# Optimization experiments

Hardware: AMD Instinct MI355X
Metric: run time of the kernel (lower is better)

Reference implementation:

```python
import math
import jax, jax.numpy as jnp
from jax import lax
import numpy as np

L, B, S, H, N = 2, 1, 2048, 1024, 16
HN = H // N
EPS = 1e-5
SIGMA = 0.02
OUT_STD = SIGMA / math.sqrt(2.0 * L)


def gelu(x):
    # OpenAI tanh-approx gelu, matching gelu_impl
    return 0.5 * x * (1.0 + jnp.tanh(0.7978845608028654 * x * (1.0 + 0.044715 * x * x)))


def layer_norm(x, g, b):
    mu = jnp.mean(x, axis=-1, keepdims=True)
    var = jnp.mean(jnp.square(x - mu), axis=-1, keepdims=True)
    return (x - mu) / jnp.sqrt(var + EPS) * g + b


def setup_inputs() -> dict:
    key = jax.random.key(0)
    ks = jax.random.split(key, 8)
    x = jax.random.normal(ks[0], (B, S, H), dtype=jnp.float32)
    ltor_mask = jnp.tril(jnp.ones((S, S), dtype=jnp.float32))[None, None]  # [1,1,S,S]
    return {
        "hidden_states": x,
        "ltor_mask": ltor_mask,
        "ln1_g": jnp.ones((L, H), jnp.float32),
        "ln1_b": jnp.zeros((L, H), jnp.float32),
        "qkv_w": jax.random.normal(ks[1], (L, H, 3 * H), jnp.float32) * SIGMA,
        "qkv_b": jnp.zeros((L, 3 * H), jnp.float32),
        "dense_w": jax.random.normal(ks[2], (L, H, H), jnp.float32) * OUT_STD,
        "dense_b": jnp.zeros((L, H), jnp.float32),
        "ln2_g": jnp.ones((L, H), jnp.float32),
        "ln2_b": jnp.zeros((L, H), jnp.float32),
        "fc_w": jax.random.normal(ks[3], (L, H, 4 * H), jnp.float32) * SIGMA,
        "fc_b": jnp.zeros((L, 4 * H), jnp.float32),
        "proj_w": jax.random.normal(ks[4], (L, 4 * H, H), jnp.float32) * OUT_STD,
        "proj_b": jnp.zeros((L, H), jnp.float32),
        "lnf_g": jnp.ones((H,), jnp.float32),
        "lnf_b": jnp.zeros((H,), jnp.float32),
    }


def _transformer(hidden_states, ltor_mask, ln1_g, ln1_b, qkv_w, qkv_b, dense_w, dense_b,
                 ln2_g, ln2_b, fc_w, fc_b, proj_w, proj_b, lnf_g, lnf_b):
    scale = 1.0 / math.sqrt(HN)

    def step(h, p):
        g1, b1, qw, qb, dw, db, g2, b2, fw, fb, pw, pb = p
        y = layer_norm(h, g1, b1)
        qkv = y @ qw + qb                       # [B,S,3H]
        q, k, v = jnp.split(qkv, 3, axis=-1)
        # [B,S,H] -> [B,N,S,HN]
        q = q.reshape(B, S, N, HN).transpose(0, 2, 1, 3)
        k = k.reshape(B, S, N, HN).transpose(0, 2, 1, 3)
        v = v.reshape(B, S, N, HN).transpose(0, 2, 1, 3)
        scores = jnp.einsum('bnqd,bnkd->bnqk', q, k) * scale
        scores = scores * ltor_mask - 10000.0 * (1.0 - ltor_mask)
        probs = jax.nn.softmax(scores, axis=-1)
        ctx = jnp.einsum('bnqk,bnkd->bnqd', probs, v)
        ctx = ctx.transpose(0, 2, 1, 3).reshape(B, S, H)
        attn_out = ctx @ dw + db
        h2 = h + attn_out
        y2 = layer_norm(h2, g2, b2)
        mlp_out = gelu(y2 @ fw + fb) @ pw + pb
        return h2 + mlp_out, None

    params = (ln1_g, ln1_b, qkv_w, qkv_b, dense_w, dense_b,
              ln2_g, ln2_b, fc_w, fc_b, proj_w, proj_b)
    h, _ = lax.scan(step, hidden_states, params)
    return layer_norm(h, lnf_g, lnf_b)


def reference(hidden_states, ltor_mask, ln1_g, ln1_b, qkv_w, qkv_b, dense_w, dense_b,
              ln2_g, ln2_b, fc_w, fc_b, proj_w, proj_b, lnf_g, lnf_b):
    return _transformer(hidden_states, ltor_mask, ln1_g, ln1_b, qkv_w, qkv_b,
                        dense_w, dense_b, ln2_g, ln2_b, fc_w, fc_b,
                        proj_w, proj_b, lnf_g, lnf_b)
```

## Files before the change

kernel.cpp:

```cpp
#include <hip/hip_runtime.h>
#include <hip/hip_bf16.h>
#include <cstdint>
#include <cstddef>

typedef __bf16 bf16;
typedef __attribute__((ext_vector_type(4))) __bf16 bf16x4;
typedef __attribute__((ext_vector_type(8))) __bf16 bf16x8;
typedef __attribute__((ext_vector_type(4))) float floatx4;

__device__ __forceinline__ void gload16(const bf16* g, bf16* l) {
    __builtin_amdgcn_global_load_lds(
        (const __attribute__((address_space(1))) void*)g,
        (__attribute__((address_space(3))) void*)l, 16, 0, 0);
}

__global__ __launch_bounds__(256) void ln_first(const float* __restrict__ x,
                                                float* __restrict__ h,
                                                const float* __restrict__ g,
                                                const float* __restrict__ b,
                                                bf16* __restrict__ y) {
    __shared__ float red[8];
    const int row = blockIdx.x, tid = threadIdx.x;
    const size_t off = (size_t)row * 1024 + tid * 4;
    const float4 v = *(const float4*)(x + off);
    *(float4*)(h + off) = v;
    float s = v.x + v.y + v.z + v.w;
#pragma unroll
    for (int o = 32; o > 0; o >>= 1) s += __shfl_xor(s, o);
    if ((tid & 63) == 0) red[tid >> 6] = s;
    __syncthreads();
    const float mean = (red[0] + red[1] + red[2] + red[3]) * (1.f / 1024.f);
    const float d[4] = {v.x - mean, v.y - mean, v.z - mean, v.w - mean};
    float q = d[0] * d[0] + d[1] * d[1] + d[2] * d[2] + d[3] * d[3];
#pragma unroll
    for (int o = 32; o > 0; o >>= 1) q += __shfl_xor(q, o);
    if ((tid & 63) == 0) red[4 + (tid >> 6)] = q;
    __syncthreads();
    const float var = (red[4] + red[5] + red[6] + red[7]) * (1.f / 1024.f);
    const float rstd = rsqrtf(var + 1e-5f);
    const int base = tid * 4;
#pragma unroll
    for (int i = 0; i < 4; i++)
        y[off + i] = (bf16)(d[i] * rstd * g[base + i] + b[base + i]);
}

template <typename OutT, int KS>
__global__ __launch_bounds__(256) void reduce_ln(const bf16* __restrict__ part,
                                                 const float* __restrict__ bias,
                                                 float* __restrict__ h,
                                                 const float* __restrict__ g,
                                                 const float* __restrict__ b,
                                                 OutT* __restrict__ y) {
    __shared__ float red[8];
    const int row = blockIdx.x, tid = threadIdx.x;
    const int base = tid * 4;
    const size_t off = (size_t)row * 1024 + base;
    const float4 hv = *(const float4*)(h + off);
    const float4 bv = *(const float4*)(bias + base);
    float a[4] = {hv.x + bv.x, hv.y + bv.y, hv.z + bv.z, hv.w + bv.w};
#pragma unroll
    for (int z = 0; z < KS; z++) {
        bf16x4 pv = *(const bf16x4*)(part + (size_t)z * (2048 * 1024) + off);
#pragma unroll
        for (int i = 0; i < 4; i++) a[i] += (float)pv[i];
    }
    *(float4*)(h + off) = (float4){a[0], a[1], a[2], a[3]};
    float s = a[0] + a[1] + a[2] + a[3];
#pragma unroll
    for (int o = 32; o > 0; o >>= 1) s += __shfl_xor(s, o);
    if ((tid & 63) == 0) red[tid >> 6] = s;
    __syncthreads();
    const float mean = (red[0] + red[1] + red[2] + red[3]) * (1.f / 1024.f);
    const float d[4] = {a[0] - mean, a[1] - mean, a[2] - mean, a[3] - mean};
    float q = d[0] * d[0] + d[1] * d[1] + d[2] * d[2] + d[3] * d[3];
#pragma unroll
    for (int o = 32; o > 0; o >>= 1) q += __shfl_xor(q, o);
    if ((tid & 63) == 0) red[4 + (tid >> 6)] = q;
    __syncthreads();
    const float var = (red[4] + red[5] + red[6] + red[7]) * (1.f / 1024.f);
    const float rstd = rsqrtf(var + 1e-5f);
#pragma unroll
    for (int i = 0; i < 4; i++)
        y[off + i] = (OutT)(d[i] * rstd * g[base + i] + b[base + i]);
}

__global__ __launch_bounds__(256) void transpose_all(const float* __restrict__ qkv_w,
                                                     const float* __restrict__ dense_w,
                                                     const float* __restrict__ fc_w,
                                                     const float* __restrict__ proj_w,
                                                     bf16* __restrict__ wT) {
    __shared__ bf16 T[128][72];
    int b = blockIdx.x;
    const int layer = (b >= 1536) ? 1 : 0;
    b -= layer * 1536;
    const float* src; bf16* dst; int K, N, kx, ny;
    bf16* wl = wT + (size_t)layer * 12582912;
    if (b < 384)       { src = qkv_w  + (size_t)layer * 1024 * 3072; dst = wl;            K = 1024; N = 3072; kx = b & 7;  ny = b >> 3; }
    else if (b < 512)  { b -= 384;  src = dense_w + (size_t)layer * 1024 * 1024; dst = wl + 3145728; K = 1024; N = 1024; kx = b & 7;  ny = b >> 3; }
    else if (b < 1024) { b -= 512;  src = fc_w    + (size_t)layer * 1024 * 4096; dst = wl + 4194304; K = 1024; N = 4096; kx = b & 7;  ny = b >> 3; }
    else               { b -= 1024; src = proj_w  + (size_t)layer * 4096 * 1024; dst = wl + 8388608; K = 4096; N = 1024; kx = b & 31; ny = b >> 5; }
    const int k0 = kx * 128, n0 = ny * 64;
    {
        const int r = threadIdx.x >> 4;
        const int c4 = (threadIdx.x & 15) * 4;
#pragma unroll
        for (int j = 0; j < 8; j++) {
            const int kk = r + j * 16;
            float4 v = *(const float4*)&src[(size_t)(k0 + kk) * N + n0 + c4];
            bf16x4 bv; bv[0] = (bf16)v.x; bv[1] = (bf16)v.y; bv[2] = (bf16)v.z; bv[3] = (bf16)v.w;
            *(bf16x4*)&T[kk][c4 ^ (((kk >> 5) & 3) << 4)] = bv;
        }
    }
    __syncthreads();
    {
        const int n = threadIdx.x >> 2;
        const int kc = (threadIdx.x & 3) * 32;
#pragma unroll
        for (int j = 0; j < 4; j++) {
            bf16x8 v;
#pragma unroll
            for (int i = 0; i < 8; i++) {
                const int k = kc + j * 8 + i;
                v[i] = T[k][n ^ (((k >> 5) & 3) << 4)];
            }
            *(bf16x8*)&dst[(size_t)(n0 + n) * K + k0 + kc + j * 8] = v;
        }
    }
}

template <int MODE>
__global__ __launch_bounds__(256) void gemm_bt64(const bf16* __restrict__ A,
                                                 const bf16* __restrict__ BT,
                                                 const float* __restrict__ bias,
                                                 bf16* __restrict__ outb,
                                                 int M, int N, int K) {
    __shared__ bf16 As[64 * 64];
    __shared__ bf16 Bs[128 * 64];
    const int tid = threadIdx.x;
    const int w = tid >> 6, lane = tid & 63;
    const int quad = lane >> 4, l16 = lane & 15;
    const int wm = w >> 1, wn = w & 1;
    const int m0 = blockIdx.x * 64, n0 = blockIdx.y * 128;
    const int kchunk = K / gridDim.z;
    const int kbeg = blockIdx.z * kchunk;

    const int srow = lane >> 3;
    const int scol = ((lane & 7) ^ srow) * 8;
    const bf16* ga = A + (size_t)(m0 + w * 16 + srow) * K + kbeg + scol;
    const bf16* gb = BT + (size_t)(n0 + w * 32 + srow) * K + kbeg + scol;
    bf16* la = As + (w * 16) * 64;
    bf16* lb = Bs + (w * 32) * 64;

    floatx4 acc[2][4];
#pragma unroll
    for (int i = 0; i < 2; i++)
#pragma unroll
        for (int j = 0; j < 4; j++) acc[i][j] = (floatx4){0.f, 0.f, 0.f, 0.f};

#pragma unroll
    for (int s = 0; s < 2; s++) gload16(ga + (size_t)(s * 8) * K, la + s * 8 * 64);
#pragma unroll
    for (int s = 0; s < 4; s++) gload16(gb + (size_t)(s * 8) * K, lb + s * 8 * 64);

    const int xq = (l16 & 7) * 8;

    for (int kk = 0; kk < kchunk; kk += 64) {
        __syncthreads();
        bf16x8 af[2][2], bfr[2][4];
#pragma unroll
        for (int ks = 0; ks < 2; ks++) {
            const int colz = (ks * 32 + quad * 8) ^ xq;
#pragma unroll
            for (int i = 0; i < 2; i++)
                af[ks][i]  = *(const bf16x8*)&As[(wm * 32 + i * 16 + l16) * 64 + colz];
#pragma unroll
            for (int i = 0; i < 4; i++)
                bfr[ks][i] = *(const bf16x8*)&Bs[(wn * 64 + i * 16 + l16) * 64 + colz];
        }
        __syncthreads();
        if (kk + 64 < kchunk) {
#pragma unroll
            for (int s = 0; s < 2; s++) gload16(ga + (size_t)(s * 8) * K + kk + 64, la + s * 8 * 64);
#pragma unroll
            for (int s = 0; s < 4; s++) gload16(gb + (size_t)(s * 8) * K + kk + 64, lb + s * 8 * 64);
        }
#pragma unroll
        for (int ks = 0; ks < 2; ks++)
#pragma unroll
            for (int ms = 0; ms < 2; ms++)
#pragma unroll
                for (int ns = 0; ns < 4; ns++)
                    acc[ms][ns] = __builtin_amdgcn_mfma_f32_16x16x32_bf16(af[ks][ms], bfr[ks][ns],
                                                                          acc[ms][ns], 0, 0, 0);
    }

    bf16* pout = (MODE == 2) ? (outb + (size_t)blockIdx.z * M * N) : outb;
#pragma unroll
    for (int ms = 0; ms < 2; ms++) {
#pragma unroll
        for (int ns = 0; ns < 4; ns++) {
            const int row = m0 + wm * 32 + ms * 16 + quad * 4;
            const int col = n0 + wn * 64 + ns * 16 + l16;
            const float bv = (MODE == 2) ? 0.f : bias[col];
#pragma unroll
            for (int i = 0; i < 4; i++) {
                float v = acc[ms][ns][i] + bv;
                size_t idx = (size_t)(row + i) * N + col;
                if (MODE == 1) {
                    float t = 0.7978845608028654f * v * (1.f + 0.044715f * v * v);
                    pout[idx] = (bf16)(0.5f * v * (1.f + tanhf(t)));
                } else {
                    pout[idx] = (bf16)v;
                }
            }
        }
    }
}

__global__ __launch_bounds__(256) void attn_mfma(const bf16* __restrict__ qkv,
                                                 bf16* __restrict__ ctx) {
    __shared__ bf16 Ks[64][68];
    __shared__ bf16 Vt[64][72];
    __shared__ bf16 QPa[64][68];
    __shared__ bf16 QPb[64][68];
    const int tid = threadIdx.x;
    const int w = tid >> 6, lane = tid & 63;
    const int quad = lane >> 4, l16 = lane & 15;
    const int head = blockIdx.y;
    const int qta = blockIdx.x;
    const int qtb = 31 - qta;
    const int qa = qta * 64, qb = qtb * 64;
    const int rowg = w * 16 + quad * 4;
    const int r = tid >> 2;
    const int c = (tid & 3) * 16;
    const float SC = 0.18033688011111827f;

    {
        const bf16* pa = qkv + (size_t)(qa + r) * 3072 + head * 64 + c;
        const bf16* pb = qkv + (size_t)(qb + r) * 3072 + head * 64 + c;
        bf16x8 a0 = *(const bf16x8*)pa, a1 = *(const bf16x8*)(pa + 8);
        bf16x8 b0 = *(const bf16x8*)pb, b1 = *(const bf16x8*)(pb + 8);
        bf16x8 sa0, sa1, sb0, sb1;
#pragma unroll
        for (int i = 0; i < 8; i++) {
            sa0[i] = (bf16)((float)a0[i] * SC); sa1[i] = (bf16)((float)a1[i] * SC);
            sb0[i] = (bf16)((float)b0[i] * SC); sb1[i] = (bf16)((float)b1[i] * SC);
        }
        *(bf16x8*)&QPa[r][c] = sa0; *(bf16x8*)&QPa[r][c + 8] = sa1;
        *(bf16x8*)&QPb[r][c] = sb0; *(bf16x8*)&QPb[r][c + 8] = sb1;
    }
    const bf16x8 aqA0 = *(const bf16x8*)&QPa[w * 16 + l16][quad * 8];
    const bf16x8 aqA1 = *(const bf16x8*)&QPa[w * 16 + l16][32 + quad * 8];
    const bf16x8 aqB0 = *(const bf16x8*)&QPb[w * 16 + l16][quad * 8];
    const bf16x8 aqB1 = *(const bf16x8*)&QPb[w * 16 + l16][32 + quad * 8];

    float lsa[4] = {0.f, 0.f, 0.f, 0.f}, lsb[4] = {0.f, 0.f, 0.f, 0.f};
    floatx4 oa[4], ob[4];
#pragma unroll
    for (int d = 0; d < 4; d++) {
        oa[d] = (floatx4){0.f, 0.f, 0.f, 0.f};
        ob[d] = (floatx4){0.f, 0.f, 0.f, 0.f};
    }

    const int nt = qtb + 1;
    bf16x8 kr0, kr1, vr0, vr1;
    {
        const bf16* kp = qkv + (size_t)r * 3072 + 1024 + head * 64 + c;
        kr0 = *(const bf16x8*)kp; kr1 = *(const bf16x8*)(kp + 8);
        const bf16* vp = qkv + (size_t)lane * 3072 + 2048 + head * 64 + w * 16;
        vr0 = *(const bf16x8*)vp; vr1 = *(const bf16x8*)(vp + 8);
    }

    for (int t = 0; t < nt; t++) {
        __syncthreads();
        *(bf16x8*)&Ks[r][c] = kr0;
        *(bf16x8*)&Ks[r][c + 8] = kr1;
#pragma unroll
        for (int i = 0; i < 8; i++) {
            Vt[w * 16 + i][lane] = vr0[i];
            Vt[w * 16 + 8 + i][lane] = vr1[i];
        }
        __syncthreads();
        if (t + 1 < nt) {
            const size_t kb = (size_t)(t + 1) * 64;
            const bf16* kp = qkv + (kb + r) * 3072 + 1024 + head * 64 + c;
            kr0 = *(const bf16x8*)kp; kr1 = *(const bf16x8*)(kp + 8);
            const bf16* vp = qkv + (kb + lane) * 3072 + 2048 + head * 64 + w * 16;
            vr0 = *(const bf16x8*)vp; vr1 = *(const bf16x8*)(vp + 8);
        }
        const bool doA = (t <= qta);

        floatx4 s4b[4], s4a[4];
#pragma unroll
        for (int n = 0; n < 4; n++) s4b[n] = (floatx4){0.f, 0.f, 0.f, 0.f};
#pragma unroll
        for (int n = 0; n < 4; n++) {
            bf16x8 bk0 = *(const bf16x8*)&Ks[n * 16 + l16][quad * 8];
            bf16x8 bk1 = *(const bf16x8*)&Ks[n * 16 + l16][32 + quad * 8];
            s4b[n] = __builtin_amdgcn_mfma_f32_16x16x32_bf16(aqB0, bk0, s4b[n], 0, 0, 0);
            s4b[n] = __builtin_amdgcn_mfma_f32_16x16x32_bf16(aqB1, bk1, s4b[n], 0, 0, 0);
        }
        if (doA) {
#pragma unroll
            for (int n = 0; n < 4; n++) s4a[n] = (floatx4){0.f, 0.f, 0.f, 0.f};
#pragma unroll
            for (int n = 0; n < 4; n++) {
                bf16x8 bk0 = *(const bf16x8*)&Ks[n * 16 + l16][quad * 8];
                bf16x8 bk1 = *(const bf16x8*)&Ks[n * 16 + l16][32 + quad * 8];
                s4a[n] = __builtin_amdgcn_mfma_f32_16x16x32_bf16(aqA0, bk0, s4a[n], 0, 0, 0);
                s4a[n] = __builtin_amdgcn_mfma_f32_16x16x32_bf16(aqA1, bk1, s4a[n], 0, 0, 0);
            }
        }

        {
            float p[4][4];
            if (t == nt - 1) {
#pragma unroll
                for (int i = 0; i < 4; i++)
#pragma unroll
                    for (int n = 0; n < 4; n++)
                        p[n][i] = (n * 16 + l16 > rowg + i) ? 0.f
                                  : __builtin_amdgcn_exp2f(s4b[n][i]);
            } else {
#pragma unroll
                for (int i = 0; i < 4; i++)
#pragma unroll
                    for (int n = 0; n < 4; n++)
                        p[n][i] = __builtin_amdgcn_exp2f(s4b[n][i]);
            }
#pragma unroll
            for (int i = 0; i < 4; i++)
#pragma unroll
                for (int n = 0; n < 4; n++) lsb[i] += p[n][i];
#pragma unroll
            for (int n = 0; n < 4; n++)
#pragma unroll
                for (int i = 0; i < 4; i++)
                    QPb[rowg + i][n * 16 + l16] = (bf16)p[n][i];
        }
        if (doA) {
            float p[4][4];
            if (t == qta) {
#pragma unroll
                for (int i = 0; i < 4; i++)
#pragma unroll
                    for (int n = 0; n < 4; n++)
                        p[n][i] = (n * 16 + l16 > rowg + i) ? 0.f
                                  : __builtin_amdgcn_exp2f(s4a[n][i]);
            } else {
#pragma unroll
                for (int i = 0; i < 4; i++)
#pragma unroll
                    for (int n = 0; n < 4; n++)
                        p[n][i] = __builtin_amdgcn_exp2f(s4a[n][i]);
            }
#pragma unroll
            for (int i = 0; i < 4; i++)
#pragma unroll
                for (int n = 0; n < 4; n++) lsa[i] += p[n][i];
#pragma unroll
            for (int n = 0; n < 4; n++)
#pragma unroll
                for (int i = 0; i < 4; i++)
                    QPa[rowg + i][n * 16 + l16] = (bf16)p[n][i];
        }

        {
            bf16x8 ap0 = *(const bf16x8*)&QPb[w * 16 + l16][quad * 8];
            bf16x8 ap1 = *(const bf16x8*)&QPb[w * 16 + l16][32 + quad * 8];
#pragma unroll
            for (int d = 0; d < 4; d++) {
                bf16x8 bv0 = *(const bf16x8*)&Vt[d * 16 + l16][quad * 8];
                bf16x8 bv1 = *(const bf16x8*)&Vt[d * 16 + l16][32 + quad * 8];
                ob[d] = __builtin_amdgcn_mfma_f32_16x16x32_bf16(ap0, bv0, ob[d], 0, 0, 0);
                ob[d] = __builtin_amdgcn_mfma_f32_16x16x32_bf16(ap1, bv1, ob[d], 0, 0, 0);
            }
        }
        if (doA) {
            bf16x8 ap0 = *(const bf16x8*)&QPa[w * 16 + l16][quad * 8];
            bf16x8 ap1 = *(const bf16x8*)&QPa[w * 16 + l16][32 + quad * 8];
#pragma unroll
            for (int d = 0; d < 4; d++) {
                bf16x8 bv0 = *(const bf16x8*)&Vt[d * 16 + l16][quad * 8];
                bf16x8 bv1 = *(const bf16x8*)&Vt[d * 16 + l16][32 + quad * 8];
                oa[d] = __builtin_amdgcn_mfma_f32_16x16x32_bf16(ap0, bv0, oa[d], 0, 0, 0);
                oa[d] = __builtin_amdgcn_mfma_f32_16x16x32_bf16(ap1, bv1, oa[d], 0, 0, 0);
            }
        }
    }

#pragma unroll
    for (int i = 0; i < 4; i++) {
#pragma unroll
        for (int msk = 1; msk < 16; msk <<= 1) {
            lsb[i] += __shfl_xor(lsb[i], msk);
            lsa[i] += __shfl_xor(lsa[i], msk);
        }
    }
#pragma unroll
    for (int i = 0; i < 4; i++) {
        const float rlb = 1.f / lsb[i];
        const float rla = 1.f / lsa[i];
        const size_t rbB = (size_t)(qb + rowg + i) * 1024 + head * 64;
        const size_t rbA = (size_t)(qa + rowg + i) * 1024 + head * 64;
#pragma unroll
        for (int d = 0; d < 4; d++) {
            ctx[rbB + d * 16 + l16] = (bf16)(ob[d][i] * rlb);
            ctx[rbA + d * 16 + l16] = (bf16)(oa[d][i] * rla);
        }
    }
}

extern "C" void kernel_launch(void* const* d_in, const int* in_sizes, int n_in,
                              void* d_out, int out_size, void* d_ws, size_t ws_size,
                              hipStream_t stream) {
    const float* hidden  = (const float*)d_in[0];
    const float* ln1_g   = (const float*)d_in[2];
    const float* ln1_b   = (const float*)d_in[3];
    const float* qkv_w   = (const float*)d_in[4];
    const float* qkv_b   = (const float*)d_in[5];
    const float* dense_w = (const float*)d_in[6];
    const float* dense_b = (const float*)d_in[7];
    const float* ln2_g   = (const float*)d_in[8];
    const float* ln2_b   = (const float*)d_in[9];
    const float* fc_w    = (const float*)d_in[10];
    const float* fc_b    = (const float*)d_in[11];
    const float* proj_w  = (const float*)d_in[12];
    const float* proj_b  = (const float*)d_in[13];
    const float* lnf_g   = (const float*)d_in[14];
    const float* lnf_b   = (const float*)d_in[15];

    char* ws = (char*)d_ws;
    float* h    = (float*)(ws);
    bf16* y     = (bf16*)(ws + 8u   * 1024 * 1024);
    bf16* qkvb  = (bf16*)(ws + 12u  * 1024 * 1024);
    bf16* ctx   = (bf16*)(ws + 24u  * 1024 * 1024);
    bf16* mlp   = (bf16*)(ws + 12u  * 1024 * 1024);
    bf16* part  = (bf16*)(ws + 36u  * 1024 * 1024);
    bf16* wT    = (bf16*)(ws + 52u  * 1024 * 1024);

    const size_t LW = 12582912;

    transpose_all<<<3072, 256, 0, stream>>>(qkv_w, dense_w, fc_w, proj_w, wT);
    ln_first<<<2048, 256, 0, stream>>>(hidden, h, ln1_g, ln1_b, y);

    for (int l = 0; l < 2; l++) {
        bf16* wTq = wT + (size_t)l * LW;
        bf16* wTd = wTq + 3145728;
        bf16* wTf = wTq + 4194304;
        bf16* wTp = wTq + 8388608;

        gemm_bt64<0><<<dim3(32, 24, 1), 256, 0, stream>>>(y, wTq, qkv_b + l * 3072, qkvb, 2048, 3072, 1024);
        attn_mfma<<<dim3(16, 16), 256, 0, stream>>>(qkvb, ctx);

        gemm_bt64<2><<<dim3(32, 8, 4), 256, 0, stream>>>(ctx, wTd, nullptr, part, 2048, 1024, 1024);
        reduce_ln<bf16, 4><<<2048, 256, 0, stream>>>(part, dense_b + l * 1024, h,
                                                     ln2_g + l * 1024, ln2_b + l * 1024, y);

        gemm_bt64<1><<<dim3(32, 32, 1), 256, 0, stream>>>(y, wTf, fc_b + l * 4096, mlp, 2048, 4096, 1024);
        gemm_bt64<2><<<dim3(32, 8, 4), 256, 0, stream>>>(mlp, wTp, nullptr, part, 2048, 1024, 4096);
        if (l == 0) {
            reduce_ln<bf16, 4><<<2048, 256, 0, stream>>>(part, proj_b, h,
                                                         ln1_g + 1024, ln1_b + 1024, y);
        } else {
            reduce_ln<float, 4><<<2048, 256, 0, stream>>>(part, proj_b + 1024, h,
                                                          lnf_g, lnf_b, (float*)d_out);
        }
    }
}
```

Before: 437.7 us.

## Split paired causal attention tiles into separate blocks and retile weight transpose

Attention previously paired query tile qa with its mirror 31-qa in one block to balance causal work. Now each block handles a single query tile, launched in descending order of work, which doubles the grid to 512 blocks and cuts per-block register and LDS use. The cost is less work per block and each K/V tile being loaded once per query tile instead of once per pair. Separately, the weight transpose moves from 128x64 bf16 tiles to 64x64 fp32 tiles with padding instead of an XOR swizzle, doubling its block count.

```diff
diff --git a/kernel.cpp b/kernel.cpp
--- a/kernel.cpp
+++ b/kernel.cpp
@@ -89,41 +89,37 @@
                                                      const float* __restrict__ fc_w,
                                                      const float* __restrict__ proj_w,
                                                      bf16* __restrict__ wT) {
-    __shared__ bf16 T[128][72];
+    __shared__ float T[64][65];
     int b = blockIdx.x;
-    const int layer = (b >= 1536) ? 1 : 0;
-    b -= layer * 1536;
+    const int layer = (b >= 3072) ? 1 : 0;
+    b -= layer * 3072;
     const float* src; bf16* dst; int K, N, kx, ny;
     bf16* wl = wT + (size_t)layer * 12582912;
-    if (b < 384)       { src = qkv_w  + (size_t)layer * 1024 * 3072; dst = wl;            K = 1024; N = 3072; kx = b & 7;  ny = b >> 3; }
-    else if (b < 512)  { b -= 384;  src = dense_w + (size_t)layer * 1024 * 1024; dst = wl + 3145728; K = 1024; N = 1024; kx = b & 7;  ny = b >> 3; }
-    else if (b < 1024) { b -= 512;  src = fc_w    + (size_t)layer * 1024 * 4096; dst = wl + 4194304; K = 1024; N = 4096; kx = b & 7;  ny = b >> 3; }
-    else               { b -= 1024; src = proj_w  + (size_t)layer * 4096 * 1024; dst = wl + 8388608; K = 4096; N = 1024; kx = b & 31; ny = b >> 5; }
-    const int k0 = kx * 128, n0 = ny * 64;
+    if (b < 768)       { src = qkv_w  + (size_t)layer * 1024 * 3072; dst = wl;            K = 1024; N = 3072; kx = b & 15; ny = b >> 4; }
+    else if (b < 1024) { b -= 768;  src = dense_w + (size_t)layer * 1024 * 1024; dst = wl + 3145728; K = 1024; N = 1024; kx = b & 15; ny = b >> 4; }
+    else if (b < 2048) { b -= 1024; src = fc_w    + (size_t)layer * 1024 * 4096; dst = wl + 4194304; K = 1024; N = 4096; kx = b & 15; ny = b >> 4; }
+    else               { b -= 2048; src = proj_w  + (size_t)layer * 4096 * 1024; dst = wl + 8388608; K = 4096; N = 1024; kx = b & 63; ny = b >> 6; }
+    const int k0 = kx * 64, n0 = ny * 64;
     {
         const int r = threadIdx.x >> 4;
         const int c4 = (threadIdx.x & 15) * 4;
 #pragma unroll
-        for (int j = 0; j < 8; j++) {
-            const int kk = r + j * 16;
-            float4 v = *(const float4*)&src[(size_t)(k0 + kk) * N + n0 + c4];
-            bf16x4 bv; bv[0] = (bf16)v.x; bv[1] = (bf16)v.y; bv[2] = (bf16)v.z; bv[3] = (bf16)v.w;
-            *(bf16x4*)&T[kk][c4 ^ (((kk >> 5) & 3) << 4)] = bv;
+        for (int j = 0; j < 4; j++) {
+            float4 v = *(const float4*)&src[(size_t)(k0 + r + j * 16) * N + n0 + c4];
+            T[r + j * 16][c4 + 0] = v.x; T[r + j * 16][c4 + 1] = v.y;
+            T[r + j * 16][c4 + 2] = v.z; T[r + j * 16][c4 + 3] = v.w;
         }
     }
     __syncthreads();
     {
-        const int n = threadIdx.x >> 2;
-        const int kc = (threadIdx.x & 3) * 32;
-#pragma unroll
-        for (int j = 0; j < 4; j++) {
+        const int rn = threadIdx.x >> 3;
+        const int c8 = (threadIdx.x & 7) * 8;
+#pragma unroll
+        for (int j = 0; j < 2; j++) {
             bf16x8 v;
 #pragma unroll
-            for (int i = 0; i < 8; i++) {
-                const int k = kc + j * 8 + i;
-                v[i] = T[k][n ^ (((k >> 5) & 3) << 4)];
-            }
-            *(bf16x8*)&dst[(size_t)(n0 + n) * K + k0 + kc + j * 8] = v;
+            for (int i = 0; i < 8; i++) v[i] = (bf16)T[c8 + i][rn + j * 32];
+            *(bf16x8*)&dst[(size_t)(n0 + rn + j * 32) * K + k0 + c8] = v;
         }
     }
 }
@@ -221,48 +217,37 @@
                                                  bf16* __restrict__ ctx) {
     __shared__ bf16 Ks[64][68];
     __shared__ bf16 Vt[64][72];
-    __shared__ bf16 QPa[64][68];
-    __shared__ bf16 QPb[64][68];
+    __shared__ bf16 QP[64][68];
     const int tid = threadIdx.x;
     const int w = tid >> 6, lane = tid & 63;
     const int quad = lane >> 4, l16 = lane & 15;
     const int head = blockIdx.y;
-    const int qta = blockIdx.x;
-    const int qtb = 31 - qta;
-    const int qa = qta * 64, qb = qtb * 64;
+    const int qt = 31 - blockIdx.x;
+    const int q0 = qt * 64;
     const int rowg = w * 16 + quad * 4;
     const int r = tid >> 2;
     const int c = (tid & 3) * 16;
     const float SC = 0.18033688011111827f;
 
     {
-        const bf16* pa = qkv + (size_t)(qa + r) * 3072 + head * 64 + c;
-        const bf16* pb = qkv + (size_t)(qb + r) * 3072 + head * 64 + c;
-        bf16x8 a0 = *(const bf16x8*)pa, a1 = *(const bf16x8*)(pa + 8);
-        bf16x8 b0 = *(const bf16x8*)pb, b1 = *(const bf16x8*)(pb + 8);
-        bf16x8 sa0, sa1, sb0, sb1;
+        const bf16* pq = qkv + (size_t)(q0 + r) * 3072 + head * 64 + c;
+        bf16x8 a0 = *(const bf16x8*)pq, a1 = *(const bf16x8*)(pq + 8);
+        bf16x8 s0, s1;
 #pragma unroll
         for (int i = 0; i < 8; i++) {
-            sa0[i] = (bf16)((float)a0[i] * SC); sa1[i] = (bf16)((float)a1[i] * SC);
-            sb0[i] = (bf16)((float)b0[i] * SC); sb1[i] = (bf16)((float)b1[i] * SC);
-        }
-        *(bf16x8*)&QPa[r][c] = sa0; *(bf16x8*)&QPa[r][c + 8] = sa1;
-        *(bf16x8*)&QPb[r][c] = sb0; *(bf16x8*)&QPb[r][c + 8] = sb1;
-    }
-    const bf16x8 aqA0 = *(const bf16x8*)&QPa[w * 16 + l16][quad * 8];
-    const bf16x8 aqA1 = *(const bf16x8*)&QPa[w * 16 + l16][32 + quad * 8];
-    const bf16x8 aqB0 = *(const bf16x8*)&QPb[w * 16 + l16][quad * 8];
-    const bf16x8 aqB1 = *(const bf16x8*)&QPb[w * 16 + l16][32 + quad * 8];
-
-    float lsa[4] = {0.f, 0.f, 0.f, 0.f}, lsb[4] = {0.f, 0.f, 0.f, 0.f};
-    floatx4 oa[4], ob[4];
-#pragma unroll
-    for (int d = 0; d < 4; d++) {
-        oa[d] = (floatx4){0.f, 0.f, 0.f, 0.f};
-        ob[d] = (floatx4){0.f, 0.f, 0.f, 0.f};
-    }
-
-    const int nt = qtb + 1;
+            s0[i] = (bf16)((float)a0[i] * SC); s1[i] = (bf16)((float)a1[i] * SC);
+        }
+        *(bf16x8*)&QP[r][c] = s0; *(bf16x8*)&QP[r][c + 8] = s1;
+    }
+    const bf16x8 aq0 = *(const bf16x8*)&QP[w * 16 + l16][quad * 8];
+    const bf16x8 aq1 = *(const bf16x8*)&QP[w * 16 + l16][32 + quad * 8];
+
+    float ls[4] = {0.f, 0.f, 0.f, 0.f};
+    floatx4 o[4];
+#pragma unroll
+    for (int d = 0; d < 4; d++) o[d] = (floatx4){0.f, 0.f, 0.f, 0.f};
+
+    const int nt = qt + 1;
     bf16x8 kr0, kr1, vr0, vr1;
     {
         const bf16* kp = qkv + (size_t)r * 3072 + 1024 + head * 64 + c;
@@ -288,28 +273,16 @@
             const bf16* vp = qkv + (kb + lane) * 3072 + 2048 + head * 64 + w * 16;
             vr0 = *(const bf16x8*)vp; vr1 = *(const bf16x8*)(vp + 8);
         }
-        const bool doA = (t <= qta);
-
-        floatx4 s4b[4], s4a[4];
-#pragma unroll
-        for (int n = 0; n < 4; n++) s4b[n] = (floatx4){0.f, 0.f, 0.f, 0.f};
+
+        floatx4 s4[4];
+#pragma unroll
+        for (int n = 0; n < 4; n++) s4[n] = (floatx4){0.f, 0.f, 0.f, 0.f};
 #pragma unroll
         for (int n = 0; n < 4; n++) {
             bf16x8 bk0 = *(const bf16x8*)&Ks[n * 16 + l16][quad * 8];
             bf16x8 bk1 = *(const bf16x8*)&Ks[n * 16 + l16][32 + quad * 8];
-            s4b[n] = __builtin_amdgcn_mfma_f32_16x16x32_bf16(aqB0, bk0, s4b[n], 0, 0, 0);
-            s4b[n] = __builtin_amdgcn_mfma_f32_16x16x32_bf16(aqB1, bk1, s4b[n], 0, 0, 0);
-        }
-        if (doA) {
-#pragma unroll
-            for (int n = 0; n < 4; n++) s4a[n] = (floatx4){0.f, 0.f, 0.f, 0.f};
-#pragma unroll
-            for (int n = 0; n < 4; n++) {
-                bf16x8 bk0 = *(const bf16x8*)&Ks[n * 16 + l16][quad * 8];
-                bf16x8 bk1 = *(const bf16x8*)&Ks[n * 16 + l16][32 + quad * 8];
-                s4a[n] = __builtin_amdgcn_mfma_f32_16x16x32_bf16(aqA0, bk0, s4a[n], 0, 0, 0);
-                s4a[n] = __builtin_amdgcn_mfma_f32_16x16x32_bf16(aqA1, bk1, s4a[n], 0, 0, 0);
-            }
+            s4[n] = __builtin_amdgcn_mfma_f32_16x16x32_bf16(aq0, bk0, s4[n], 0, 0, 0);
+            s4[n] = __builtin_amdgcn_mfma_f32_16x16x32_bf16(aq1, bk1, s4[n], 0, 0, 0);
         }
 
         {
@@ -320,94 +293,51 @@
 #pragma unroll
                     for (int n = 0; n < 4; n++)
                         p[n][i] = (n * 16 + l16 > rowg + i) ? 0.f
-                                  : __builtin_amdgcn_exp2f(s4b[n][i]);
+                                  : __builtin_amdgcn_exp2f(s4[n][i]);
             } else {
 #pragma unroll
                 for (int i = 0; i < 4; i++)
 #pragma unroll
                     for (int n = 0; n < 4; n++)
-                        p[n][i] = __builtin_amdgcn_exp2f(s4b[n][i]);
+                        p[n][i] = __builtin_amdgcn_exp2f(s4[n][i]);
             }
 #pragma unroll
             for (int i = 0; i < 4; i++)
 #pragma unroll
-                for (int n = 0; n < 4; n++) lsb[i] += p[n][i];
+                for (int n = 0; n < 4; n++) ls[i] += p[n][i];
 #pragma unroll
             for (int n = 0; n < 4; n++)
 #pragma unroll
                 for (int i = 0; i < 4; i++)
-                    QPb[rowg + i][n * 16 + l16] = (bf16)p[n][i];
-        }
-        if (doA) {
-            float p[4][4];
-            if (t == qta) {
-#pragma unroll
-                for (int i = 0; i < 4; i++)
-#pragma unroll
-                    for (int n = 0; n < 4; n++)
-                        p[n][i] = (n * 16 + l16 > rowg + i) ? 0.f
-                                  : __builtin_amdgcn_exp2f(s4a[n][i]);
-            } else {
-#pragma unroll
-                for (int i = 0; i < 4; i++)
-#pragma unroll
-                    for (int n = 0; n < 4; n++)
-                        p[n][i] = __builtin_amdgcn_exp2f(s4a[n][i]);
-            }
-#pragma unroll
-            for (int i = 0; i < 4; i++)
-#pragma unroll
-                for (int n = 0; n < 4; n++) lsa[i] += p[n][i];
-#pragma unroll
-            for (int n = 0; n < 4; n++)
-#pragma unroll
-                for (int i = 0; i < 4; i++)
-                    QPa[rowg + i][n * 16 + l16] = (bf16)p[n][i];
+                    QP[rowg + i][n * 16 + l16] = (bf16)p[n][i];
         }
 
         {
-            bf16x8 ap0 = *(const bf16x8*)&QPb[w * 16 + l16][quad * 8];
-            bf16x8 ap1 = *(const bf16x8*)&QPb[w * 16 + l16][32 + quad * 8];
+            bf16x8 ap0 = *(const bf16x8*)&QP[w * 16 + l16][quad * 8];
+            bf16x8 ap1 = *(const bf16x8*)&QP[w * 16 + l16][32 + quad * 8];
 #pragma unroll
             for (int d = 0; d < 4; d++) {
                 bf16x8 bv0 = *(const bf16x8*)&Vt[d * 16 + l16][quad * 8];
                 bf16x8 bv1 = *(const bf16x8*)&Vt[d * 16 + l16][32 + quad * 8];
-                ob[d] = __builtin_amdgcn_mfma_f32_16x16x32_bf16(ap0, bv0, ob[d], 0, 0, 0);
-                ob[d] = __builtin_amdgcn_mfma_f32_16x16x32_bf16(ap1, bv1, ob[d], 0, 0, 0);
+                o[d] = __builtin_amdgcn_mfma_f32_16x16x32_bf16(ap0, bv0, o[d], 0, 0, 0);
+                o[d] = __builtin_amdgcn_mfma_f32_16x16x32_bf16(ap1, bv1, o[d], 0, 0, 0);
             }
         }
-        if (doA) {
-            bf16x8 ap0 = *(const bf16x8*)&QPa[w * 16 + l16][quad * 8];
-            bf16x8 ap1 = *(const bf16x8*)&QPa[w * 16 + l16][32 + quad * 8];
-#pragma unroll
-            for (int d = 0; d < 4; d++) {
-                bf16x8 bv0 = *(const bf16x8*)&Vt[d * 16 + l16][quad * 8];
-                bf16x8 bv1 = *(const bf16x8*)&Vt[d * 16 + l16][32 + quad * 8];
-                oa[d] = __builtin_amdgcn_mfma_f32_16x16x32_bf16(ap0, bv0, oa[d], 0, 0, 0);
-                oa[d] = __builtin_amdgcn_mfma_f32_16x16x32_bf16(ap1, bv1, oa[d], 0, 0, 0);
-            }
-        }
     }
 
 #pragma unroll
     for (int i = 0; i < 4; i++) {
 #pragma unroll
-        for (int msk = 1; msk < 16; msk <<= 1) {
-            lsb[i] += __shfl_xor(lsb[i], msk);
-            lsa[i] += __shfl_xor(lsa[i], msk);
-        }
+        for (int msk = 1; msk < 16; msk <<= 1)
+            ls[i] += __shfl_xor(ls[i], msk);
     }
 #pragma unroll
     for (int i = 0; i < 4; i++) {
-        const float rlb = 1.f / lsb[i];
-        const float rla = 1.f / lsa[i];
-        const size_t rbB = (size_t)(qb + rowg + i) * 1024 + head * 64;
-        const size_t rbA = (size_t)(qa + rowg + i) * 1024 + head * 64;
-#pragma unroll
-        for (int d = 0; d < 4; d++) {
-            ctx[rbB + d * 16 + l16] = (bf16)(ob[d][i] * rlb);
-            ctx[rbA + d * 16 + l16] = (bf16)(oa[d][i] * rla);
-        }
+        const float rl = 1.f / ls[i];
+        const size_t rb = (size_t)(q0 + rowg + i) * 1024 + head * 64;
+#pragma unroll
+        for (int d = 0; d < 4; d++)
+            ctx[rb + d * 16 + l16] = (bf16)(o[d][i] * rl);
     }
 }
 
@@ -441,7 +371,7 @@
 
     const size_t LW = 12582912;
 
-    transpose_all<<<3072, 256, 0, stream>>>(qkv_w, dense_w, fc_w, proj_w, wT);
+    transpose_all<<<6144, 256, 0, stream>>>(qkv_w, dense_w, fc_w, proj_w, wT);
     ln_first<<<2048, 256, 0, stream>>>(hidden, h, ln1_g, ln1_b, y);
 
     for (int l = 0; l < 2; l++) {
@@ -451,7 +381,7 @@
         bf16* wTp = wTq + 8388608;
 
         gemm_bt64<0><<<dim3(32, 24, 1), 256, 0, stream>>>(y, wTq, qkv_b + l * 3072, qkvb, 2048, 3072, 1024);
-        attn_mfma<<<dim3(16, 16), 256, 0, stream>>>(qkvb, ctx);
+        attn_mfma<<<dim3(32, 16), 256, 0, stream>>>(qkvb, ctx);
 
         gemm_bt64<2><<<dim3(32, 8, 4), 256, 0, stream>>>(ctx, wTd, nullptr, part, 2048, 1024, 1024);
         reduce_ln<bf16, 4><<<2048, 256, 0, stream>>>(part, dense_b + l * 1024, h,
```

New measurement: 458.0 us. +4.6%, slower.
